# Optimization experiments

Hardware: AMD Instinct MI355X
Metric: run time of the kernel (lower is better)

## Reference

```python
import jax, jax.numpy as jnp
import numpy as np

ALPHA = 32
R = 16
SCALING = ALPHA / R  # 2.0


def setup_inputs() -> dict:
    key = jax.random.key(0)
    k1, k2, k3, k4 = jax.random.split(key, 4)
    B_, S, D = 4, 2048, 4096
    H, r, O = 8, R, 4096
    x = jax.random.normal(k1, (B_, S, D), dtype=jnp.float32)
    A = jax.random.normal(k2, (H, r, D), dtype=jnp.float32) * 0.02   # down-proj per head
    Bm = jax.random.normal(k3, (H, O, r), dtype=jnp.float32) * 0.02  # up-proj per head
    Wr = jax.random.normal(k4, (H, D), dtype=jnp.float32) * 0.02     # router weight
    br = jnp.zeros((H,), dtype=jnp.float32)                          # router bias
    return {"x": x, "A": A, "B": Bm, "Wr": Wr, "br": br}


def reference(x, A, B, Wr, br):
    H = A.shape[0]
    # Router: logits [b, s, h], scores scaled by num_heads
    router_logits = jnp.einsum('bsd,hd->bsh', x, Wr) + br
    scores = H * jax.nn.softmax(router_logits, axis=-1)
    # Per-head low-rank projection: [b, s, h, r]
    low = jnp.einsum('bsd,hrd->bshr', x, A)
    # Fused up-projection + router-weighted combine over heads: [b, s, o]
    out = jnp.einsum('bshr,hor,bsh->bso', low, B, scores)
    return SCALING * out
```

## Files before the change

### kernel.cpp

```cpp
#include <hip/hip_runtime.h>
#include <math.h>

#define D_DIM 4096
#define O_DIM 4096
#define KSPLIT 8

typedef __attribute__((ext_vector_type(8))) short short8;
typedef __attribute__((ext_vector_type(4))) float floatx4;

__device__ inline unsigned short f2bf(float f) {
    union { float f; unsigned u; } v; v.f = f;
    unsigned r = v.u + 0x7FFF + ((v.u >> 16) & 1);
    return (unsigned short)(r >> 16);
}

__global__ __launch_bounds__(256) void k0a_prepW1(const float* __restrict__ A,
                                                  const float* __restrict__ Wr,
                                                  unsigned short* __restrict__ W1bf) {
    int e = (blockIdx.x * 256 + threadIdx.x) * 4;
    int row = e >> 12;
    int col = e & 4095;
    float4 v;
    if (row < 128)      v = *(const float4*)(A + (size_t)row * D_DIM + col);
    else if (row < 136) v = *(const float4*)(Wr + (size_t)(row - 128) * D_DIM + col);
    else                v = make_float4(0.f, 0.f, 0.f, 0.f);
    ushort4 o; o.x = f2bf(v.x); o.y = f2bf(v.y); o.z = f2bf(v.z); o.w = f2bf(v.w);
    *(ushort4*)(W1bf + e) = o;
}

__global__ __launch_bounds__(256) void k0b_prepBt(const float* __restrict__ B,
                                                  unsigned short* __restrict__ Btbf) {
    int e = (blockIdx.x * 256 + threadIdx.x) * 4;
    int o = e >> 7;
    int k = e & 127;
    int h = k >> 4;
    int r = k & 15;
    float4 v = *(const float4*)(B + (size_t)h * (O_DIM * 16) + (size_t)o * 16 + r);
    ushort4 w; w.x = f2bf(v.x); w.y = f2bf(v.y); w.z = f2bf(v.z); w.w = f2bf(v.w);
    *(ushort4*)(Btbf + e) = w;
}

__global__ __launch_bounds__(256) void k1_gemm1(const float* __restrict__ X,
                                                const unsigned short* __restrict__ W1bf,
                                                float* __restrict__ P) {
    __shared__ short Xs[64][72];
    __shared__ short Ws[144][72];
    const int kslice = blockIdx.x & (KSPLIT - 1);
    const int mblk   = blockIdx.x >> 3;
    const int m0     = mblk * 64;
    const int kbase  = kslice * (D_DIM / KSPLIT);
    const int tid  = threadIdx.x;
    const int wave = tid >> 6;
    const int lane = tid & 63;
    const int lrow = lane & 15;
    const int quad = lane >> 4;

    floatx4 acc[9];
    #pragma unroll
    for (int n = 0; n < 9; ++n) acc[n] = (floatx4)(0.f);

    for (int it = 0; it < (D_DIM / KSPLIT) / 64; ++it) {
        const int k0c = kbase + it * 64;
        #pragma unroll
        for (int i = 0; i < 4; ++i) {
            int e   = tid + i * 256;
            int row = e >> 4;
            int c4  = e & 15;
            float4 v = *(const float4*)(X + (size_t)(m0 + row) * D_DIM + k0c + c4 * 4);
            ushort4 o; o.x = f2bf(v.x); o.y = f2bf(v.y); o.z = f2bf(v.z); o.w = f2bf(v.w);
            *(ushort4*)&Xs[row][c4 * 4] = o;
        }
        #pragma unroll
        for (int i = 0; i < 5; ++i) {
            int e = tid + i * 256;
            if (e < 1152) {
                int row = e >> 3;
                int c8  = e & 7;
                uint4 v = *(const uint4*)(W1bf + (size_t)row * D_DIM + k0c + c8 * 8);
                *(uint4*)&Ws[row][c8 * 8] = v;
            }
        }
        __syncthreads();
        #pragma unroll
        for (int ks = 0; ks < 2; ++ks) {
            const int koff = ks * 32 + quad * 8;
            short8 a = *(const short8*)&Xs[wave * 16 + lrow][koff];
            #pragma unroll
            for (int n = 0; n < 9; ++n) {
                short8 b = *(const short8*)&Ws[n * 16 + lrow][koff];
                acc[n] = __builtin_amdgcn_mfma_f32_16x16x32_bf16(a, b, acc[n], 0, 0, 0);
            }
        }
        __syncthreads();
    }

    float* Pk = P + (size_t)kslice * (8192 * 144);
    #pragma unroll
    for (int n = 0; n < 9; ++n) {
        #pragma unroll
        for (int reg = 0; reg < 4; ++reg) {
            int row = m0 + wave * 16 + quad * 4 + reg;
            int col = n * 16 + lrow;
            Pk[(size_t)row * 144 + col] = acc[n][reg];
        }
    }
}

__global__ __launch_bounds__(256) void k15_reduce_softmax(const float* __restrict__ P,
                                                          const float* __restrict__ br,
                                                          unsigned short* __restrict__ W2) {
    __shared__ float S[16][148];
    const int t0  = blockIdx.x * 16;
    const int tid = threadIdx.x;
    #pragma unroll
    for (int i = 0; i < 3; ++i) {
        int e = tid + i * 256;
        if (e < 576) {
            int row = e / 36;
            int c4  = e - row * 36;
            size_t off = (size_t)(t0 + row) * 144 + c4 * 4;
            float4 s = *(const float4*)(P + off);
            #pragma unroll
            for (int p = 1; p < KSPLIT; ++p) {
                float4 v = *(const float4*)(P + (size_t)p * (8192 * 144) + off);
                s.x += v.x; s.y += v.y; s.z += v.z; s.w += v.w;
            }
            *(float4*)&S[row][c4 * 4] = s;
        }
    }
    __syncthreads();
    if (tid < 16) {
        float l[8]; float m = -1e30f;
        #pragma unroll
        for (int h = 0; h < 8; ++h) { l[h] = S[tid][128 + h] + br[h]; m = fmaxf(m, l[h]); }
        float s = 0.f;
        #pragma unroll
        for (int h = 0; h < 8; ++h) { l[h] = __expf(l[h] - m); s += l[h]; }
        float inv = 16.0f / s;
        #pragma unroll
        for (int h = 0; h < 8; ++h) S[tid][136 + h] = l[h] * inv;
    }
    __syncthreads();
    #pragma unroll
    for (int i = 0; i < 2; ++i) {
        int e   = tid + i * 256;
        int tok = e >> 5;
        int c4  = e & 31;
        int col = c4 * 4;
        float sc = S[tok][136 + (col >> 4)];
        ushort4 o;
        o.x = f2bf(S[tok][col + 0] * sc);
        o.y = f2bf(S[tok][col + 1] * sc);
        o.z = f2bf(S[tok][col + 2] * sc);
        o.w = f2bf(S[tok][col + 3] * sc);
        *(ushort4*)(W2 + (size_t)(t0 + tok) * 128 + col) = o;
    }
}

__global__ __launch_bounds__(256) void k2_gemm2(const unsigned short* __restrict__ W2,
                                                const unsigned short* __restrict__ Btbf,
                                                float* __restrict__ out) {
    __shared__ short Bs[128][136];
    const int nblk = blockIdx.x & 31;
    const int mblk = blockIdx.x >> 5;
    const int m0 = mblk * 128, n0 = nblk * 128;
    const int tid  = threadIdx.x;
    const int wave = tid >> 6;
    const int lane = tid & 63;
    const int lrow = lane & 15;
    const int quad = lane >> 4;

    #pragma unroll
    for (int i = 0; i < 8; ++i) {
        int e   = tid + i * 256;
        int row = e >> 4;
        int c8  = e & 15;
        *(uint4*)&Bs[row][c8 * 8] = *(const uint4*)(Btbf + (size_t)(n0 + row) * 128 + c8 * 8);
    }
    __syncthreads();

    floatx4 acc[2][8];
    #pragma unroll
    for (int i = 0; i < 2; ++i)
        #pragma unroll
        for (int n = 0; n < 8; ++n) acc[i][n] = (floatx4)(0.f);

    #pragma unroll
    for (int ks = 0; ks < 4; ++ks) {
        const int koff = ks * 32 + quad * 8;
        short8 a[2];
        #pragma unroll
        for (int i = 0; i < 2; ++i)
            a[i] = *(const short8*)(W2 + (size_t)(m0 + wave * 32 + i * 16 + lrow) * 128 + koff);
        #pragma unroll
        for (int n = 0; n < 8; ++n) {
            short8 b = *(const short8*)&Bs[n * 16 + lrow][koff];
            #pragma unroll
            for (int i = 0; i < 2; ++i)
                acc[i][n] = __builtin_amdgcn_mfma_f32_16x16x32_bf16(a[i], b, acc[i][n], 0, 0, 0);
        }
    }

    #pragma unroll
    for (int i = 0; i < 2; ++i) {
        #pragma unroll
        for (int n = 0; n < 8; ++n) {
            #pragma unroll
            for (int reg = 0; reg < 4; ++reg) {
                int row = m0 + wave * 32 + i * 16 + quad * 4 + reg;
                int col = n0 + n * 16 + lrow;
                __builtin_nontemporal_store(acc[i][n][reg], out + (size_t)row * O_DIM + col);
            }
        }
    }
}

extern "C" void kernel_launch(void* const* d_in, const int* in_sizes, int n_in,
                              void* d_out, int out_size, void* d_ws, size_t ws_size,
                              hipStream_t stream) {
    const float* x  = (const float*)d_in[0];
    const float* A  = (const float*)d_in[1];
    const float* B  = (const float*)d_in[2];
    const float* Wr = (const float*)d_in[3];
    const float* br = (const float*)d_in[4];
    float* out = (float*)d_out;

    float* ws = (float*)d_ws;
    float*          P     = ws;
    unsigned short* W2    = (unsigned short*)(ws + 9437184);
    unsigned short* W1bf  = (unsigned short*)(ws + 9437184 + 524288);
    unsigned short* Btbf  = (unsigned short*)(ws + 9437184 + 524288 + 294912);

    k0a_prepW1<<<dim3(576), dim3(256), 0, stream>>>(A, Wr, W1bf);
    k0b_prepBt<<<dim3(512), dim3(256), 0, stream>>>(B, Btbf);
    k1_gemm1<<<dim3(128 * KSPLIT), dim3(256), 0, stream>>>(x, W1bf, P);
    k15_reduce_softmax<<<dim3(512), dim3(256), 0, stream>>>(P, br, W2);
    k2_gemm2<<<dim3(64 * 32), dim3(256), 0, stream>>>(W2, Btbf, out);
}
```

Before: 289.2 us.

## Enlarge gemm1 M tile, merge prep kernels, stage gemm2 output via LDS

Three changes at once. The gemm1 M tile grows from 64 to 128 rows, so each block reuses its loaded weight tile for twice as many rows and half as many blocks are launched; X conversion now uses packed bf16x2 intrinsics. The two weight-prep kernels become one launch. gemm2's epilogue writes accumulators to shared memory and then issues coalesced 16-byte nontemporal stores, replacing scattered 4-byte stores, at the cost of extra LDS traffic and barriers.

```diff
diff --git a/kernel.cpp b/kernel.cpp
--- a/kernel.cpp
+++ b/kernel.cpp
@@ -1,4 +1,5 @@
 #include <hip/hip_runtime.h>
+#include <hip/hip_bf16.h>
 #include <math.h>
 
 #define D_DIM 4096
@@ -14,40 +15,47 @@
     return (unsigned short)(r >> 16);
 }
 
-__global__ __launch_bounds__(256) void k0a_prepW1(const float* __restrict__ A,
-                                                  const float* __restrict__ Wr,
-                                                  unsigned short* __restrict__ W1bf) {
-    int e = (blockIdx.x * 256 + threadIdx.x) * 4;
-    int row = e >> 12;
-    int col = e & 4095;
-    float4 v;
-    if (row < 128)      v = *(const float4*)(A + (size_t)row * D_DIM + col);
-    else if (row < 136) v = *(const float4*)(Wr + (size_t)(row - 128) * D_DIM + col);
-    else                v = make_float4(0.f, 0.f, 0.f, 0.f);
-    ushort4 o; o.x = f2bf(v.x); o.y = f2bf(v.y); o.z = f2bf(v.z); o.w = f2bf(v.w);
-    *(ushort4*)(W1bf + e) = o;
-}
-
-__global__ __launch_bounds__(256) void k0b_prepBt(const float* __restrict__ B,
-                                                  unsigned short* __restrict__ Btbf) {
-    int e = (blockIdx.x * 256 + threadIdx.x) * 4;
-    int o = e >> 7;
-    int k = e & 127;
-    int h = k >> 4;
-    int r = k & 15;
-    float4 v = *(const float4*)(B + (size_t)h * (O_DIM * 16) + (size_t)o * 16 + r);
-    ushort4 w; w.x = f2bf(v.x); w.y = f2bf(v.y); w.z = f2bf(v.z); w.w = f2bf(v.w);
-    *(ushort4*)(Btbf + e) = w;
+__device__ inline unsigned cvt2(float lo, float hi) {
+    __hip_bfloat162 h2 = __float22bfloat162_rn(make_float2(lo, hi));
+    union { __hip_bfloat162 h; unsigned u; } c; c.h = h2;
+    return c.u;
+}
+
+__global__ __launch_bounds__(256) void k0_prep(const float* __restrict__ A,
+                                               const float* __restrict__ Wr,
+                                               const float* __restrict__ B,
+                                               unsigned short* __restrict__ W1bf,
+                                               unsigned short* __restrict__ Btbf) {
+    if (blockIdx.x < 576) {
+        int e = (blockIdx.x * 256 + threadIdx.x) * 4;
+        int row = e >> 12;
+        int col = e & 4095;
+        float4 v;
+        if (row < 128)      v = *(const float4*)(A + (size_t)row * D_DIM + col);
+        else if (row < 136) v = *(const float4*)(Wr + (size_t)(row - 128) * D_DIM + col);
+        else                v = make_float4(0.f, 0.f, 0.f, 0.f);
+        ushort4 o; o.x = f2bf(v.x); o.y = f2bf(v.y); o.z = f2bf(v.z); o.w = f2bf(v.w);
+        *(ushort4*)(W1bf + e) = o;
+    } else {
+        int e = ((blockIdx.x - 576) * 256 + threadIdx.x) * 4;
+        int o = e >> 7;
+        int k = e & 127;
+        int h = k >> 4;
+        int r = k & 15;
+        float4 v = *(const float4*)(B + (size_t)h * (O_DIM * 16) + (size_t)o * 16 + r);
+        ushort4 w; w.x = f2bf(v.x); w.y = f2bf(v.y); w.z = f2bf(v.z); w.w = f2bf(v.w);
+        *(ushort4*)(Btbf + e) = w;
+    }
 }
 
 __global__ __launch_bounds__(256) void k1_gemm1(const float* __restrict__ X,
                                                 const unsigned short* __restrict__ W1bf,
                                                 float* __restrict__ P) {
-    __shared__ short Xs[64][72];
+    __shared__ short Xs[128][72];
     __shared__ short Ws[144][72];
     const int kslice = blockIdx.x & (KSPLIT - 1);
     const int mblk   = blockIdx.x >> 3;
-    const int m0     = mblk * 64;
+    const int m0     = mblk * 128;
     const int kbase  = kslice * (D_DIM / KSPLIT);
     const int tid  = threadIdx.x;
     const int wave = tid >> 6;
@@ -55,20 +63,22 @@
     const int lrow = lane & 15;
     const int quad = lane >> 4;
 
-    floatx4 acc[9];
-    #pragma unroll
-    for (int n = 0; n < 9; ++n) acc[n] = (floatx4)(0.f);
+    floatx4 acc[2][9];
+    #pragma unroll
+    for (int i = 0; i < 2; ++i)
+        #pragma unroll
+        for (int n = 0; n < 9; ++n) acc[i][n] = (floatx4)(0.f);
 
     for (int it = 0; it < (D_DIM / KSPLIT) / 64; ++it) {
         const int k0c = kbase + it * 64;
         #pragma unroll
-        for (int i = 0; i < 4; ++i) {
+        for (int i = 0; i < 8; ++i) {
             int e   = tid + i * 256;
             int row = e >> 4;
             int c4  = e & 15;
             float4 v = *(const float4*)(X + (size_t)(m0 + row) * D_DIM + k0c + c4 * 4);
-            ushort4 o; o.x = f2bf(v.x); o.y = f2bf(v.y); o.z = f2bf(v.z); o.w = f2bf(v.w);
-            *(ushort4*)&Xs[row][c4 * 4] = o;
+            uint2 o; o.x = cvt2(v.x, v.y); o.y = cvt2(v.z, v.w);
+            *(uint2*)&Xs[row][c4 * 4] = o;
         }
         #pragma unroll
         for (int i = 0; i < 5; ++i) {
@@ -84,11 +94,16 @@
         #pragma unroll
         for (int ks = 0; ks < 2; ++ks) {
             const int koff = ks * 32 + quad * 8;
-            short8 a = *(const short8*)&Xs[wave * 16 + lrow][koff];
+            short8 a[2];
+            #pragma unroll
+            for (int i = 0; i < 2; ++i)
+                a[i] = *(const short8*)&Xs[wave * 32 + i * 16 + lrow][koff];
             #pragma unroll
             for (int n = 0; n < 9; ++n) {
                 short8 b = *(const short8*)&Ws[n * 16 + lrow][koff];
-                acc[n] = __builtin_amdgcn_mfma_f32_16x16x32_bf16(a, b, acc[n], 0, 0, 0);
+                #pragma unroll
+                for (int i = 0; i < 2; ++i)
+                    acc[i][n] = __builtin_amdgcn_mfma_f32_16x16x32_bf16(a[i], b, acc[i][n], 0, 0, 0);
             }
         }
         __syncthreads();
@@ -96,12 +111,15 @@
 
     float* Pk = P + (size_t)kslice * (8192 * 144);
     #pragma unroll
-    for (int n = 0; n < 9; ++n) {
-        #pragma unroll
-        for (int reg = 0; reg < 4; ++reg) {
-            int row = m0 + wave * 16 + quad * 4 + reg;
-            int col = n * 16 + lrow;
-            Pk[(size_t)row * 144 + col] = acc[n][reg];
+    for (int i = 0; i < 2; ++i) {
+        #pragma unroll
+        for (int n = 0; n < 9; ++n) {
+            #pragma unroll
+            for (int reg = 0; reg < 4; ++reg) {
+                int row = m0 + wave * 32 + i * 16 + quad * 4 + reg;
+                int col = n * 16 + lrow;
+                Pk[(size_t)row * 144 + col] = acc[i][n][reg];
+            }
         }
     }
 }
@@ -160,7 +178,10 @@
 __global__ __launch_bounds__(256) void k2_gemm2(const unsigned short* __restrict__ W2,
                                                 const unsigned short* __restrict__ Btbf,
                                                 float* __restrict__ out) {
-    __shared__ short Bs[128][136];
+    __shared__ union {
+        short Bs[128][136];
+        float Sf[64][132];
+    } sm;
     const int nblk = blockIdx.x & 31;
     const int mblk = blockIdx.x >> 5;
     const int m0 = mblk * 128, n0 = nblk * 128;
@@ -175,7 +196,7 @@
         int e   = tid + i * 256;
         int row = e >> 4;
         int c8  = e & 15;
-        *(uint4*)&Bs[row][c8 * 8] = *(const uint4*)(Btbf + (size_t)(n0 + row) * 128 + c8 * 8);
+        *(uint4*)&sm.Bs[row][c8 * 8] = *(const uint4*)(Btbf + (size_t)(n0 + row) * 128 + c8 * 8);
     }
     __syncthreads();
 
@@ -194,24 +215,36 @@
             a[i] = *(const short8*)(W2 + (size_t)(m0 + wave * 32 + i * 16 + lrow) * 128 + koff);
         #pragma unroll
         for (int n = 0; n < 8; ++n) {
-            short8 b = *(const short8*)&Bs[n * 16 + lrow][koff];
+            short8 b = *(const short8*)&sm.Bs[n * 16 + lrow][koff];
             #pragma unroll
             for (int i = 0; i < 2; ++i)
                 acc[i][n] = __builtin_amdgcn_mfma_f32_16x16x32_bf16(a[i], b, acc[i][n], 0, 0, 0);
         }
     }
-
-    #pragma unroll
-    for (int i = 0; i < 2; ++i) {
-        #pragma unroll
-        for (int n = 0; n < 8; ++n) {
-            #pragma unroll
-            for (int reg = 0; reg < 4; ++reg) {
-                int row = m0 + wave * 32 + i * 16 + quad * 4 + reg;
-                int col = n0 + n * 16 + lrow;
-                __builtin_nontemporal_store(acc[i][n][reg], out + (size_t)row * O_DIM + col);
-            }
-        }
+    __syncthreads();
+
+    #pragma unroll
+    for (int h = 0; h < 2; ++h) {
+        if ((wave >> 1) == h) {
+            #pragma unroll
+            for (int i = 0; i < 2; ++i)
+                #pragma unroll
+                for (int n = 0; n < 8; ++n)
+                    #pragma unroll
+                    for (int reg = 0; reg < 4; ++reg)
+                        sm.Sf[(wave & 1) * 32 + i * 16 + quad * 4 + reg][n * 16 + lrow] = acc[i][n][reg];
+        }
+        __syncthreads();
+        #pragma unroll
+        for (int i2 = 0; i2 < 8; ++i2) {
+            int e   = tid + i2 * 256;
+            int row = e >> 5;
+            int c4  = e & 31;
+            floatx4 v = *(const floatx4*)&sm.Sf[row][c4 * 4];
+            __builtin_nontemporal_store(v,
+                (floatx4*)(out + (size_t)(m0 + h * 64 + row) * O_DIM + n0 + c4 * 4));
+        }
+        __syncthreads();
     }
 }
 
@@ -231,9 +264,8 @@
     unsigned short* W1bf  = (unsigned short*)(ws + 9437184 + 524288);
     unsigned short* Btbf  = (unsigned short*)(ws + 9437184 + 524288 + 294912);
 
-    k0a_prepW1<<<dim3(576), dim3(256), 0, stream>>>(A, Wr, W1bf);
-    k0b_prepBt<<<dim3(512), dim3(256), 0, stream>>>(B, Btbf);
-    k1_gemm1<<<dim3(128 * KSPLIT), dim3(256), 0, stream>>>(x, W1bf, P);
+    k0_prep<<<dim3(1088), dim3(256), 0, stream>>>(A, Wr, B, W1bf, Btbf);
+    k1_gemm1<<<dim3(64 * KSPLIT), dim3(256), 0, stream>>>(x, W1bf, P);
     k15_reduce_softmax<<<dim3(512), dim3(256), 0, stream>>>(P, br, W2);
     k2_gemm2<<<dim3(64 * 32), dim3(256), 0, stream>>>(W2, Btbf, out);
 }
```

New measurement: 270.7 us. 1.07x faster.
